# Optimization experiments

Hardware: AMD Instinct MI355X
Metric: run time of the kernel (lower is better)

## Reference

```python
import jax, jax.numpy as jnp
import numpy as np


def setup_inputs() -> dict:
    key = jax.random.key(0)
    inp = jax.random.normal(key, (8, 3, 224, 224), dtype=jnp.float32)
    return {"inp": inp, "tau_min": 1, "tau_max": 60, "ntau": 8,
            "num_angles": 12, "stride": 2}


def _logpolar_offsets(tau_min, tau_max, ntau, num_angles):
    # Matches the torch module: theta in [-pi, pi), tau logarithmically spaced,
    # coords stacked angle-major as (y, x) pairs (theta unsqueeze(1) outer).
    c = (tau_max / tau_min) ** (1.0 / (ntau - 1)) - 1.0
    theta = np.arange(num_angles, dtype=np.float64) * (2.0 * np.pi / num_angles) - np.pi
    tau = tau_min * (1.0 + c) ** np.arange(ntau, dtype=np.float64)
    x = tau[None, :] * np.cos(theta[:, None])   # (A, T)
    y = tau[None, :] * np.sin(theta[:, None])   # (A, T)
    return (jnp.asarray(y.ravel(), jnp.float32),
            jnp.asarray(x.ravel(), jnp.float32))  # each (A*T,)


def reference(inp, tau_min, tau_max, ntau, num_angles, stride):
    yoff, xoff = _logpolar_offsets(tau_min, tau_max, ntau, num_angles)
    B, F, H, W = inp.shape
    Hs = (H - 1) // stride + 1
    Ws = (W - 1) // stride + 1
    gy = jnp.arange(Hs, dtype=jnp.float32) * stride   # focus-point rows
    gx = jnp.arange(Ws, dtype=jnp.float32) * stride   # focus-point cols

    def sample(yo, xo):
        # Bilinear sample of inp at (i*stride + yo, j*stride + xo), zero outside.
        yq = gy + yo
        xq = gx + xo
        y0 = jnp.floor(yq)
        x0 = jnp.floor(xq)
        wy = (yq - y0)  # (Hs,)
        wx = (xq - x0)  # (Ws,)
        y0i = y0.astype(jnp.int32)
        x0i = x0.astype(jnp.int32)

        def gather(yi, xi):
            vy = ((yi >= 0) & (yi < H)).astype(inp.dtype)
            vx = ((xi >= 0) & (xi < W)).astype(inp.dtype)
            g = inp[:, :, jnp.clip(yi, 0, H - 1), :][:, :, :, jnp.clip(xi, 0, W - 1)]
            return g * (vy[:, None] * vx[None, :])  # (B,F,Hs,Ws)

        w00 = (1 - wy)[:, None] * (1 - wx)[None, :]
        w01 = (1 - wy)[:, None] * wx[None, :]
        w10 = wy[:, None] * (1 - wx)[None, :]
        w11 = wy[:, None] * wx[None, :]
        return (w00 * gather(y0i, x0i) + w01 * gather(y0i, x0i + 1)
                + w10 * gather(y0i + 1, x0i) + w11 * gather(y0i + 1, x0i + 1))

    out = jax.vmap(sample)(yoff, xoff)                    # (A*T, B, F, Hs, Ws)
    out = out.reshape(num_angles, ntau, B, F, Hs, Ws)
    out = jnp.transpose(out, (2, 3, 1, 0, 4, 5))          # (B, F, ntau, A, Hs, Ws)
    return out
```

## Files before the change

kernel.cpp:

```cpp
#include <hip/hip_runtime.h>
#include <cmath>
#include <algorithm>
#include <cstdint>

#ifndef M_PI
#define M_PI 3.14159265358979323846
#endif

#define B_ 8
#define F_ 3
#define H_ 224
#define W_ 224
#define T_ 8
#define A_ 12
#define NK 96
#define HS_ 112
#define WS_ 112
#define PLANE_ (H_ * W_)
#define SLICE_ (HS_ * WS_)

#define RI 8
#define BANDROWS 78
#define NLANE 56
#define PH4 56
#define PITCH4 224

struct LPArgs {
    int   cy[NK];  int cx[NK];
    float fy[NK];  float fx[NK];
    int   korig[NK];
    int   cymin[2]; int cymax[2];
};

static LPArgs make_args() {
    int cy[NK], cx[NK]; float fy[NK], fx[NK];
    double c = pow(60.0, 1.0 / 7.0) - 1.0;
    for (int t = 0; t < T_; ++t) {
        double tau = pow(1.0 + c, (double)t);
        for (int a = 0; a < A_; ++a) {
            double th = (double)a * (2.0 * M_PI / (double)A_) - M_PI;
            float yo = (float)(tau * sin(th)), xo = (float)(tau * cos(th));
            int k = t * A_ + a;
            float yf = floorf(yo), xf = floorf(xo);
            cy[k] = (int)yf; fy[k] = yo - yf;
            cx[k] = (int)xf; fx[k] = xo - xf;
        }
    }
    int idx[NK];
    for (int k = 0; k < NK; ++k) idx[k] = k;
    std::sort(idx, idx + NK, [&](int a, int b) { return cy[a] < cy[b]; });
    LPArgs r;
    r.cymin[0] = r.cymin[1] = 1000; r.cymax[0] = r.cymax[1] = -1000;
    for (int p = 0; p < NK; ++p) {
        int k = idx[p], g = p / 48;
        r.cy[p] = cy[k]; r.cx[p] = cx[k];
        r.fy[p] = fy[k]; r.fx[p] = fx[k];
        r.korig[p] = k;
        r.cymin[g] = std::min(r.cymin[g], cy[k]);
        r.cymax[g] = std::max(r.cymax[g], cy[k]);
    }
    return r;
}

typedef __attribute__((address_space(3))) unsigned int       lds_u32;
typedef __attribute__((address_space(1))) const unsigned int glb_u32;
static __device__ __forceinline__ void async_copy16(const void* g, void* l) {
    __builtin_amdgcn_global_load_lds((glb_u32*)g, (lds_u32*)l, 16, 0, 0);
}

__global__ __launch_bounds__(256) void lp_permute_kernel(
    const float* __restrict__ inp, float* __restrict__ P) {
    const int q = (int)blockIdx.x * 256 + (int)threadIdx.x;
    const float4 v = ((const float4*)inp)[q];
    const int bfr = q / PH4;
    const int u   = q - bfr * PH4;
    float* row = P + (size_t)bfr * PITCH4;
    row[u]           = v.x;
    row[PH4 + u]     = v.y;
    row[2 * PH4 + u] = v.z;
    row[3 * PH4 + u] = v.w;
}

__global__ __launch_bounds__(1024, 8) void lp_main_kernel(
    const float* __restrict__ P, float* __restrict__ out, LPArgs args) {

    __shared__ float lds[BANDROWS * PITCH4];

    const int bf = blockIdx.x;
    const int i0 = blockIdx.y * RI;
    const int g  = blockIdx.z;

    const int r0 = max(0, 2 * i0 + args.cymin[g]);
    const int r1 = min(H_ - 1, 2 * i0 + 2 * (RI - 1) + args.cymax[g] + 1);
    const int nrows = min(r1 - r0 + 1, BANDROWS);

    const int lane = threadIdx.x & 63;
    const int wave = __builtin_amdgcn_readfirstlane((int)threadIdx.x >> 6);

    const float* src = P + (size_t)bf * PLANE_ + (size_t)r0 * PITCH4;
    const int Db = nrows * (PITCH4 * 4);
    const int C  = Db >> 10;
    for (int c = wave; c < C; c += 16)
        async_copy16(src + c * 256 + lane * 4, (char*)lds + (c << 10));
    const int tail4 = (Db - (C << 10)) >> 4;
    for (int t = threadIdx.x; t < tail4; t += 1024)
        ((float4*)lds)[(C << 6) + t] = ((const float4*)src)[(C << 6) + t];
    __syncthreads();

    float* outp = out + (size_t)bf * (NK * SLICE_) + (size_t)i0 * WS_;
    const bool act = (lane < NLANE);

#pragma unroll 1
    for (int tt = 0; tt < 3; ++tt) {
        const int kk = g * 48 + wave + (tt << 4);

        const int   cy = args.cy[kk]; const float fy = args.fy[kk];
        const int   cx = args.cx[kk]; const float fx = args.fx[kk];
        const int   ko = args.korig[kk];
        const float omfx = 1.0f - fx;

        const int l = lane;
        const float* tp[4];
        float tw[4];
#pragma unroll
        for (int t = 0; t < 4; ++t) {
            const int s  = cx + t;
            const int ct = 4 * l + s;
            const int ph = s & 3;
            int idx = l + (s >> 2);
            idx = min(max(idx, 0), PH4 - 1);
            tp[t] = lds + ph * PH4 + idx;
            tw[t] = (ct >= 0 && ct < W_) ? ((t & 1) ? fx : omfx) : 0.0f;
        }

        float2* orow = (float2*)(outp + (size_t)ko * SLICE_) + l;

        if (act) {
#pragma unroll 2
            for (int di = 0; di < RI; ++di) {
                const int iy0 = 2 * (i0 + di) + cy;
                float mA, mB;
                if (iy0 >= 0 && iy0 <= H_ - 2)  { mA = 1.0f - fy; mB = fy; }
                else if (iy0 == -1)             { mA = fy;        mB = 0.0f; }
                else if (iy0 == H_ - 1)         { mA = 0.0f;      mB = 1.0f - fy; }
                else                            { mA = 0.0f;      mB = 0.0f; }
                const int by = min(max(iy0, 0), H_ - 2);
                const int rb = min(by - r0, BANDROWS - 2) * PITCH4;

                const float a0 = tp[0][rb], a1 = tp[0][rb + PITCH4];
                const float b0 = tp[1][rb], b1 = tp[1][rb + PITCH4];
                const float c0 = tp[2][rb], c1 = tp[2][rb + PITCH4];
                const float d0 = tp[3][rb], d1 = tp[3][rb + PITCH4];

                float2 rr;
                rr.x = mA * (tw[0] * a0 + tw[1] * b0)
                     + mB * (tw[0] * a1 + tw[1] * b1);
                rr.y = mA * (tw[2] * c0 + tw[3] * d0)
                     + mB * (tw[2] * c1 + tw[3] * d1);

                orow[(size_t)di * (WS_ / 2)] = rr;
            }
        }
    }
}

#define FPH 57
#define FPITCH 228
__global__ __launch_bounds__(1024, 8) void lp_fallback_kernel(
    const float* __restrict__ inp, float* __restrict__ out, LPArgs args) {

    __shared__ float lds[BANDROWS * FPITCH];

    const int bf = blockIdx.x;
    const int i0 = blockIdx.y * RI;
    const int g  = blockIdx.z;

    const int r0 = max(0, 2 * i0 + args.cymin[g]);
    const int r1 = min(H_ - 1, 2 * i0 + 2 * (RI - 1) + args.cymax[g] + 1);
    const int nrows = min(r1 - r0 + 1, BANDROWS);

    const float* plane = inp + (size_t)bf * PLANE_;
    {
        const int n = nrows * (W_ / 4);
        for (int v = threadIdx.x; v < n; v += 1024) {
            const unsigned r = (unsigned)v / 56u;
            const int u = v - (int)r * 56;
            const float4 val = *(const float4*)(plane + (size_t)(r0 + (int)r) * W_ + 4 * u);
            float* rowp = lds + r * FPITCH + u;
            rowp[0 * FPH] = val.x; rowp[1 * FPH] = val.y;
            rowp[2 * FPH] = val.z; rowp[3 * FPH] = val.w;
        }
    }
    __syncthreads();

    const int lane = threadIdx.x & 63;
    const int wave = __builtin_amdgcn_readfirstlane((int)threadIdx.x >> 6);
    float* outp = out + (size_t)bf * (NK * SLICE_) + (size_t)i0 * WS_;
    const bool act = (lane < NLANE);

#pragma unroll 1
    for (int tt = 0; tt < 3; ++tt) {
        const int kk = g * 48 + wave + (tt << 4);
        const int   cy = args.cy[kk]; const float fy = args.fy[kk];
        const int   cx = args.cx[kk]; const float fx = args.fx[kk];
        const int   ko = args.korig[kk];
        const float omfx = 1.0f - fx;
        const int l = lane;
        const float* tp[4]; float tw[4];
#pragma unroll
        for (int t = 0; t < 4; ++t) {
            const int s = cx + t; const int ct = 4 * l + s; const int ph = s & 3;
            int idx = l + (s >> 2);
            idx = min(max(idx, 0), NLANE - 1);
            tp[t] = lds + ph * FPH + idx;
            tw[t] = (ct >= 0 && ct < W_) ? ((t & 1) ? fx : omfx) : 0.0f;
        }
        float2* orow = (float2*)(outp + (size_t)ko * SLICE_) + l;
        if (act) {
#pragma unroll 2
            for (int di = 0; di < RI; ++di) {
                const int iy0 = 2 * (i0 + di) + cy;
                float mA, mB;
                if (iy0 >= 0 && iy0 <= H_ - 2)  { mA = 1.0f - fy; mB = fy; }
                else if (iy0 == -1)             { mA = fy;        mB = 0.0f; }
                else if (iy0 == H_ - 1)         { mA = 0.0f;      mB = 1.0f - fy; }
                else                            { mA = 0.0f;      mB = 0.0f; }
                const int by = min(max(iy0, 0), H_ - 2);
                const int rb = min(by - r0, BANDROWS - 2) * FPITCH;
                const float a0 = tp[0][rb], a1 = tp[0][rb + FPITCH];
                const float b0 = tp[1][rb], b1 = tp[1][rb + FPITCH];
                const float c0 = tp[2][rb], c1 = tp[2][rb + FPITCH];
                const float d0 = tp[3][rb], d1 = tp[3][rb + FPITCH];
                float2 rr;
                rr.x = mA * (tw[0] * a0 + tw[1] * b0) + mB * (tw[0] * a1 + tw[1] * b1);
                rr.y = mA * (tw[2] * c0 + tw[3] * d0) + mB * (tw[2] * c1 + tw[3] * d1);
                orow[(size_t)di * (WS_ / 2)] = rr;
            }
        }
    }
}

extern "C" void kernel_launch(void* const* d_in, const int* in_sizes, int n_in,
                              void* d_out, int out_size, void* d_ws, size_t ws_size,
                              hipStream_t stream) {
    const float* inp = (const float*)d_in[0];
    float*       out = (float*)d_out;

    static const LPArgs args = make_args();

    const size_t needP = (size_t)B_ * F_ * PLANE_ * sizeof(float);
    if (d_ws != nullptr && ws_size >= needP) {
        float* P = (float*)d_ws;
        lp_permute_kernel<<<dim3((B_ * F_ * PLANE_ / 4) / 256), 256, 0, stream>>>(inp, P);
        lp_main_kernel<<<dim3(B_ * F_, HS_ / RI, 2), 1024, 0, stream>>>(P, out, args);
    } else {
        lp_fallback_kernel<<<dim3(B_ * F_, HS_ / RI, 2), 1024, 0, stream>>>(inp, out, args);
    }
}
```

Before: 136.4 us.

## Replace LDS-banded main kernel with per-offset direct global gather kernel

Swaps the 1024-thread kernel, which staged a band of rows into LDS and looped over 48 offsets per block, for a 256-thread kernel with one block per (plane, offset, 16-row strip). Each thread reads the permuted input straight from global memory through L1/L2. The blocks are swizzled so neighbouring block IDs spread across planes. The goal is to remove the LDS staging cost and its sync, and to raise parallelism and occupancy. The price is repeated global and cache reads of overlapping rows.

```diff
diff --git a/kernel.cpp b/kernel.cpp
--- a/kernel.cpp
+++ b/kernel.cpp
@@ -19,21 +19,19 @@
 #define PLANE_ (H_ * W_)
 #define SLICE_ (HS_ * WS_)
 
-#define RI 8
-#define BANDROWS 78
-#define NLANE 56
-#define PH4 56
-#define PITCH4 224
-
-struct LPArgs {
+
+struct LPNat {
+    int   cy[NK];  int cx[NK];
+    float fy[NK];  float fx[NK];
+};
+struct LPSort {
     int   cy[NK];  int cx[NK];
     float fy[NK];  float fx[NK];
     int   korig[NK];
     int   cymin[2]; int cymax[2];
 };
 
-static LPArgs make_args() {
-    int cy[NK], cx[NK]; float fy[NK], fx[NK];
+static void host_consts(int* cy, int* cx, float* fy, float* fx) {
     double c = pow(60.0, 1.0 / 7.0) - 1.0;
     for (int t = 0; t < T_; ++t) {
         double tau = pow(1.0 + c, (double)t);
@@ -46,10 +44,21 @@
             cx[k] = (int)xf; fx[k] = xo - xf;
         }
     }
+}
+
+static LPNat make_nat() {
+    LPNat r;
+    host_consts(r.cy, r.cx, r.fy, r.fx);
+    return r;
+}
+
+static LPSort make_sort() {
+    int cy[NK], cx[NK]; float fy[NK], fx[NK];
+    host_consts(cy, cx, fy, fx);
     int idx[NK];
     for (int k = 0; k < NK; ++k) idx[k] = k;
     std::sort(idx, idx + NK, [&](int a, int b) { return cy[a] < cy[b]; });
-    LPArgs r;
+    LPSort r;
     r.cymin[0] = r.cymin[1] = 1000; r.cymax[0] = r.cymax[1] = -1000;
     for (int p = 0; p < NK; ++p) {
         int k = idx[p], g = p / 48;
@@ -62,11 +71,8 @@
     return r;
 }
 
-typedef __attribute__((address_space(3))) unsigned int       lds_u32;
-typedef __attribute__((address_space(1))) const unsigned int glb_u32;
-static __device__ __forceinline__ void async_copy16(const void* g, void* l) {
-    __builtin_amdgcn_global_load_lds((glb_u32*)g, (lds_u32*)l, 16, 0, 0);
-}
+#define PH4 56
+#define PITCH4 224
 
 __global__ __launch_bounds__(256) void lp_permute_kernel(
     const float* __restrict__ inp, float* __restrict__ P) {
@@ -81,93 +87,75 @@
     row[3 * PH4 + u] = v.w;
 }
 
-__global__ __launch_bounds__(1024, 8) void lp_main_kernel(
-    const float* __restrict__ P, float* __restrict__ out, LPArgs args) {
-
-    __shared__ float lds[BANDROWS * PITCH4];
-
-    const int bf = blockIdx.x;
-    const int i0 = blockIdx.y * RI;
-    const int g  = blockIdx.z;
-
-    const int r0 = max(0, 2 * i0 + args.cymin[g]);
-    const int r1 = min(H_ - 1, 2 * i0 + 2 * (RI - 1) + args.cymax[g] + 1);
-    const int nrows = min(r1 - r0 + 1, BANDROWS);
-
-    const int lane = threadIdx.x & 63;
-    const int wave = __builtin_amdgcn_readfirstlane((int)threadIdx.x >> 6);
-
-    const float* src = P + (size_t)bf * PLANE_ + (size_t)r0 * PITCH4;
-    const int Db = nrows * (PITCH4 * 4);
-    const int C  = Db >> 10;
-    for (int c = wave; c < C; c += 16)
-        async_copy16(src + c * 256 + lane * 4, (char*)lds + (c << 10));
-    const int tail4 = (Db - (C << 10)) >> 4;
-    for (int t = threadIdx.x; t < tail4; t += 1024)
-        ((float4*)lds)[(C << 6) + t] = ((const float4*)src)[(C << 6) + t];
-    __syncthreads();
-
-    float* outp = out + (size_t)bf * (NK * SLICE_) + (size_t)i0 * WS_;
-    const bool act = (lane < NLANE);
-
-#pragma unroll 1
-    for (int tt = 0; tt < 3; ++tt) {
-        const int kk = g * 48 + wave + (tt << 4);
-
-        const int   cy = args.cy[kk]; const float fy = args.fy[kk];
-        const int   cx = args.cx[kk]; const float fx = args.fx[kk];
-        const int   ko = args.korig[kk];
-        const float omfx = 1.0f - fx;
-
-        const int l = lane;
-        const float* tp[4];
-        float tw[4];
+__global__ __launch_bounds__(256, 8) void lp_pg_kernel(
+    const float* __restrict__ P, float* __restrict__ out, LPNat args) {
+
+    const int blk = (int)blockIdx.x;
+    const int swz = (blk & 7) * 2016 + (blk >> 3);
+    const int bf  = swz / 672;
+    const int rem = swz - bf * 672;
+    const int k   = rem / 7;
+    const int ib  = rem - k * 7;
+    const int i0  = ib * 16;
+
+    const int lane = (int)threadIdx.x & 63;
+    const int wave = (int)threadIdx.x >> 6;
+
+    const int   cy = args.cy[k]; const float fy = args.fy[k];
+    const int   cx = args.cx[k]; const float fx = args.fx[k];
+    const float omfx = 1.0f - fx;
+
+    const float* Pp = P + (size_t)bf * PLANE_;
+
+    const int l = lane;
+    int   off[4]; float tw[4];
 #pragma unroll
-        for (int t = 0; t < 4; ++t) {
-            const int s  = cx + t;
-            const int ct = 4 * l + s;
-            const int ph = s & 3;
-            int idx = l + (s >> 2);
-            idx = min(max(idx, 0), PH4 - 1);
-            tp[t] = lds + ph * PH4 + idx;
-            tw[t] = (ct >= 0 && ct < W_) ? ((t & 1) ? fx : omfx) : 0.0f;
-        }
-
-        float2* orow = (float2*)(outp + (size_t)ko * SLICE_) + l;
-
-        if (act) {
-#pragma unroll 2
-            for (int di = 0; di < RI; ++di) {
-                const int iy0 = 2 * (i0 + di) + cy;
-                float mA, mB;
-                if (iy0 >= 0 && iy0 <= H_ - 2)  { mA = 1.0f - fy; mB = fy; }
-                else if (iy0 == -1)             { mA = fy;        mB = 0.0f; }
-                else if (iy0 == H_ - 1)         { mA = 0.0f;      mB = 1.0f - fy; }
-                else                            { mA = 0.0f;      mB = 0.0f; }
-                const int by = min(max(iy0, 0), H_ - 2);
-                const int rb = min(by - r0, BANDROWS - 2) * PITCH4;
-
-                const float a0 = tp[0][rb], a1 = tp[0][rb + PITCH4];
-                const float b0 = tp[1][rb], b1 = tp[1][rb + PITCH4];
-                const float c0 = tp[2][rb], c1 = tp[2][rb + PITCH4];
-                const float d0 = tp[3][rb], d1 = tp[3][rb + PITCH4];
-
-                float2 rr;
-                rr.x = mA * (tw[0] * a0 + tw[1] * b0)
-                     + mB * (tw[0] * a1 + tw[1] * b1);
-                rr.y = mA * (tw[2] * c0 + tw[3] * d0)
-                     + mB * (tw[2] * c1 + tw[3] * d1);
-
-                orow[(size_t)di * (WS_ / 2)] = rr;
-            }
-        }
-    }
-}
-
+    for (int t = 0; t < 4; ++t) {
+        const int s  = cx + t;
+        const int ct = 4 * l + s;
+        int u = l + (s >> 2);
+        u = min(max(u, 0), PH4 - 1);
+        off[t] = (s & 3) * PH4 + u;
+        tw[t]  = (ct >= 0 && ct < W_) ? ((t & 1) ? fx : omfx) : 0.0f;
+    }
+
+    const bool act = (l < PH4);
+    float* obase = out + ((size_t)bf * NK + k) * SLICE_
+                       + (size_t)i0 * WS_ + 2 * l;
+
+#pragma unroll
+    for (int r = 0; r < 4; ++r) {
+        const int di  = wave + 4 * r;
+        const int iy0 = 2 * (i0 + di) + cy;
+        float mA, mB;
+        if (iy0 >= 0 && iy0 <= H_ - 2)  { mA = 1.0f - fy; mB = fy; }
+        else if (iy0 == -1)             { mA = fy;        mB = 0.0f; }
+        else if (iy0 == H_ - 1)         { mA = 0.0f;      mB = 1.0f - fy; }
+        else                            { mA = 0.0f;      mB = 0.0f; }
+        const int by = min(max(iy0, 0), H_ - 2);
+
+        const float* pa = Pp + (size_t)by * PITCH4;
+        const float* pb = pa + PITCH4;
+        const float a0 = pa[off[0]], b0 = pa[off[1]];
+        const float c0 = pa[off[2]], d0 = pa[off[3]];
+        const float a1 = pb[off[0]], b1 = pb[off[1]];
+        const float c1 = pb[off[2]], d1 = pb[off[3]];
+
+        float2 rr;
+        rr.x = mA * (tw[0] * a0 + tw[1] * b0) + mB * (tw[0] * a1 + tw[1] * b1);
+        rr.y = mA * (tw[2] * c0 + tw[3] * d0) + mB * (tw[2] * c1 + tw[3] * d1);
+
+        if (act) *(float2*)(obase + (size_t)di * WS_) = rr;
+    }
+}
+
+#define RI 8
+#define BANDROWS 78
 #define FPH 57
 #define FPITCH 228
+#define NLANE 56
 __global__ __launch_bounds__(1024, 8) void lp_fallback_kernel(
-    const float* __restrict__ inp, float* __restrict__ out, LPArgs args) {
+    const float* __restrict__ inp, float* __restrict__ out, LPSort args) {
 
     __shared__ float lds[BANDROWS * FPITCH];
 
@@ -246,14 +234,14 @@
     const float* inp = (const float*)d_in[0];
     float*       out = (float*)d_out;
 
-    static const LPArgs args = make_args();
-
     const size_t needP = (size_t)B_ * F_ * PLANE_ * sizeof(float);
     if (d_ws != nullptr && ws_size >= needP) {
+        static const LPNat nat = make_nat();
         float* P = (float*)d_ws;
         lp_permute_kernel<<<dim3((B_ * F_ * PLANE_ / 4) / 256), 256, 0, stream>>>(inp, P);
-        lp_main_kernel<<<dim3(B_ * F_, HS_ / RI, 2), 1024, 0, stream>>>(P, out, args);
+        lp_pg_kernel<<<dim3(24 * 96 * 7), 256, 0, stream>>>(P, out, nat);
     } else {
-        lp_fallback_kernel<<<dim3(B_ * F_, HS_ / RI, 2), 1024, 0, stream>>>(inp, out, args);
-    }
-}
+        static const LPSort srt = make_sort();
+        lp_fallback_kernel<<<dim3(B_ * F_, HS_ / RI, 2), 1024, 0, stream>>>(inp, out, srt);
+    }
+}
```

Result: slower. 139.3 us (+2.1%).
